# Optimization experiments

Measured on AMD Instinct MI355X. Metric: run time of the kernel, lower is better.

Reference implementation:

```python
import jax, jax.numpy as jnp
import numpy as np

B, T, D, H = 64, 1024, 1024, 1024  # batch, n_steps, n_in, n_hidden


def setup_inputs() -> dict:
    key = jax.random.key(0)
    k1, k2 = jax.random.split(key)
    x = jax.random.normal(k1, (B, T, D), dtype=jnp.float32)
    # BasicRNNCell kernel: [n_in + n_hidden, n_hidden], glorot-ish scale
    W = jax.random.normal(k2, (D + H, H), dtype=jnp.float32) * (1.0 / np.sqrt(D + H))
    b = jnp.zeros((H,), dtype=jnp.float32)
    return {"x": x, "W": W, "b": b}


def reference(x, W, b):
    """Vanilla RNN (tf BasicRNNCell): h_t = tanh([x_t, h_{t-1}] @ W + b).
    return_last=False -> outputs all hidden states, shape [B, T, H]."""
    Wx = W[: x.shape[-1]]   # [D, H]
    Wh = W[x.shape[-1]:]    # [H, H]
    # Precompute input projections for all steps in one big GEMM: [B, T, H]
    x_proj = jnp.einsum('btd,dh->bth', x, Wx) + b

    def step(h, xp_t):
        h_new = jnp.tanh(xp_t + h @ Wh)
        return h_new, h_new

    h0 = jnp.zeros((x.shape[0], Wh.shape[1]), dtype=x.dtype)
    # scan over time: [T, B, H]
    _, outs = jax.lax.scan(step, h0, jnp.swapaxes(x_proj, 0, 1))
    return jnp.swapaxes(outs, 0, 1)  # [B, T, H]
```

## Files before the change

kernel.cpp:

```cpp
#include <hip/hip_runtime.h>
#include <stdint.h>


#define T_LEN 1024
#define HID   1024

typedef float  f32x4  __attribute__((ext_vector_type(4)));
typedef __bf16 bf16x8 __attribute__((ext_vector_type(8)));
typedef unsigned long long u64;

__global__ __launch_bounds__(256) void xproj_gemm(
    const float* __restrict__ x, const float* __restrict__ W,
    const float* __restrict__ bias, float* __restrict__ out)
{
    __shared__ __align__(16) __bf16 As[128][40];
    __shared__ __align__(16) __bf16 Bs[128][40];

    const int bid = blockIdx.x;
    const int n0  = (bid & 7) << 7;
    const int64_t r0 = (int64_t)(bid >> 3) << 7;
    const int tid  = threadIdx.x;
    const int lane = tid & 63;
    const int w    = tid >> 6;
    const int hi   = lane >> 4, lo = lane & 15;
    const int wm   = (w >> 1) << 6, wn = (w & 1) << 6;

    f32x4 acc[4][4] = {};

    const int arow = tid >> 1, akh = (tid & 1) << 4;
    const int bk   = tid >> 3, bnh = (tid & 7) << 4;

    for (int k0 = 0; k0 < 1024; k0 += 32) {
        {
            const float* src = x + (r0 + arow) * 1024 + k0 + akh;
            bf16x8 t0, t1;
            #pragma unroll
            for (int i2 = 0; i2 < 8; ++i2) { t0[i2] = (__bf16)src[i2]; t1[i2] = (__bf16)src[8 + i2]; }
            *(bf16x8*)&As[arow][akh]     = t0;
            *(bf16x8*)&As[arow][akh + 8] = t1;
        }
        {
            const float* src = W + (int64_t)(k0 + bk) * 1024 + n0 + bnh;
            #pragma unroll
            for (int i2 = 0; i2 < 16; ++i2) {
                int col = bnh + i2;
                Bs[col][bk ^ (((col >> 4) & 3) << 3)] = (__bf16)src[i2];
            }
        }
        __syncthreads();

        bf16x8 af[4], bfr[4];
        #pragma unroll
        for (int f = 0; f < 4; ++f)
            af[f] = *(const bf16x8*)&As[wm + f * 16 + lo][hi << 3];
        #pragma unroll
        for (int f = 0; f < 4; ++f) {
            const int cswz = (((wn >> 4) + f) & 3) << 3;
            bfr[f] = *(const bf16x8*)&Bs[wn + f * 16 + lo][(hi << 3) ^ cswz];
        }
        #pragma unroll
        for (int fm = 0; fm < 4; ++fm)
            #pragma unroll
            for (int fn = 0; fn < 4; ++fn)
                acc[fm][fn] = __builtin_amdgcn_mfma_f32_16x16x32_bf16(af[fm], bfr[fn], acc[fm][fn], 0, 0, 0);
        __syncthreads();
    }

    #pragma unroll
    for (int fm = 0; fm < 4; ++fm) {
        const int64_t mrow = r0 + wm + fm * 16 + hi * 4;
        #pragma unroll
        for (int fn = 0; fn < 4; ++fn) {
            const int col = n0 + wn + fn * 16 + lo;
            const float bv = bias[col];
            #pragma unroll
            for (int r = 0; r < 4; ++r)
                out[(mrow + r) * 1024 + col] = acc[fm][fn][r] + bv;
        }
    }
}

__device__ __forceinline__ float tanh_fast(float x) {
    float e = __builtin_amdgcn_exp2f(x * 2.885390082f);
    return 1.0f - 2.0f * __builtin_amdgcn_rcpf(e + 1.0f);
}

__global__ __launch_bounds__(512, 2) void rnn_scan(
    const float* __restrict__ W, float* __restrict__ out,
    unsigned int* __restrict__ hx)
{
    __shared__ __align__(16) unsigned char A_lds[16 * 2048];

    const int bid = blockIdx.x;
    const int ig  = bid >> 3;
    const int jg  = bid & 7;
    const int tid = threadIdx.x;
    const int lane = tid & 63;
    const int wv  = tid >> 6;
    const int hi  = lane >> 4, lo = lane & 15;

    const int col = jg * 128 + wv * 16 + lo;
    bf16x8 breg[32];
    {
        const float* wb = W + (int64_t)1024 * 1024 + col;
        #pragma unroll
        for (int kb = 0; kb < 32; ++kb) {
            const float* src = wb + (int64_t)(kb * 32 + hi * 8) * 1024;
            bf16x8 tf;
            #pragma unroll
            for (int j = 0; j < 8; ++j) tf[j] = (__bf16)src[(int64_t)j * 1024];
            breg[kb] = tf;
        }
    }

    const int srow = tid >> 5;
    const int c32  = tid & 31;
    const int slab_u64 = (ig * 16 + srow) * 512 + c32 * 16;
    const unsigned swz_w = (unsigned)((srow & 7) << 4);
    const unsigned kbyte0 = (unsigned)(c32 * 64);

    const unsigned abase = (unsigned)(lo * 2048);
    const unsigned axor  = (unsigned)((lo & 7) << 4);

    const int64_t rstride = (int64_t)T_LEN * HID;
    float* pr0 = out + (int64_t)(ig * 16 + hi * 4) * rstride + col;
    const int wr0 = (ig * 16 + hi * 4) * 1024 + col;

    for (int t = 0; t < T_LEN; ++t) {
        float xpv0 = pr0[(int64_t)t * HID];
        float xpv1 = pr0[(int64_t)t * HID + rstride];
        float xpv2 = pr0[(int64_t)t * HID + 2 * rstride];
        float xpv3 = pr0[(int64_t)t * HID + 3 * rstride];

        f32x4 accs = {0.f, 0.f, 0.f, 0.f};
        if (t > 0) {
            const unsigned int exptag = (unsigned int)t;
            const u64* bp = (const u64*)(hx + ((t - 1) & 1) * 65536) + slab_u64;
            u64 q[16];
            #pragma unroll
            for (int j = 0; j < 16; ++j)
                q[j] = __hip_atomic_load(bp + j, __ATOMIC_RELAXED, __HIP_MEMORY_SCOPE_AGENT);
            unsigned bad = 0;
            #pragma unroll
            for (int j = 0; j < 16; ++j) {
                unsigned b = (((unsigned)(q[j] >> 16) & 0xffffu) ^ exptag)
                           | (((unsigned)(q[j] >> 48)) ^ exptag);
                bad |= (b ? 1u : 0u) << j;
            }
            while (bad) {
                __builtin_amdgcn_s_sleep(1);
                #pragma unroll
                for (int j = 0; j < 16; ++j)
                    if (bad & (1u << j)) {
                        q[j] = __hip_atomic_load(bp + j, __ATOMIC_RELAXED, __HIP_MEMORY_SCOPE_AGENT);
                        if ((((unsigned)(q[j] >> 16) & 0xffffu) == exptag) &&
                            ((unsigned)(q[j] >> 48) == exptag))
                            bad &= ~(1u << j);
                    }
            }
            unsigned dw[16];
            #pragma unroll
            for (int j = 0; j < 16; ++j)
                dw[j] = __builtin_amdgcn_perm((unsigned)(q[j] >> 32), (unsigned)q[j], 0x05040100u);
            #pragma unroll
            for (int i = 0; i < 4; ++i) {
                f32x4 v = { __builtin_bit_cast(float, dw[4 * i]),
                            __builtin_bit_cast(float, dw[4 * i + 1]),
                            __builtin_bit_cast(float, dw[4 * i + 2]),
                            __builtin_bit_cast(float, dw[4 * i + 3]) };
                *(f32x4*)(A_lds + srow * 2048 + ((kbyte0 + 16 * i) ^ swz_w)) = v;
            }
            __syncthreads();

            f32x4 acc0 = {0.f, 0.f, 0.f, 0.f}, acc1 = {0.f, 0.f, 0.f, 0.f};
            #pragma unroll
            for (int kb = 0; kb < 32; kb += 2) {
                bf16x8 a0 = *(const bf16x8*)(A_lds + abase + (((unsigned)(kb * 64) + hi * 16) ^ axor));
                bf16x8 a1 = *(const bf16x8*)(A_lds + abase + (((unsigned)((kb + 1) * 64) + hi * 16) ^ axor));
                acc0 = __builtin_amdgcn_mfma_f32_16x16x32_bf16(a0, breg[kb],     acc0, 0, 0, 0);
                acc1 = __builtin_amdgcn_mfma_f32_16x16x32_bf16(a1, breg[kb + 1], acc1, 0, 0, 0);
            }
            accs = acc0 + acc1;
        }

        float h0 = tanh_fast(xpv0 + accs[0]);
        float h1 = tanh_fast(xpv1 + accs[1]);
        float h2 = tanh_fast(xpv2 + accs[2]);
        float h3 = tanh_fast(xpv3 + accs[3]);

        unsigned int* hxs = hx + (t & 1) * 65536 + wr0;
        const unsigned int tagw = (unsigned int)(t + 1) << 16;
        __hip_atomic_store(hxs,        tagw | __builtin_bit_cast(unsigned short, (__bf16)h0),
                           __ATOMIC_RELAXED, __HIP_MEMORY_SCOPE_AGENT);
        __hip_atomic_store(hxs + 1024, tagw | __builtin_bit_cast(unsigned short, (__bf16)h1),
                           __ATOMIC_RELAXED, __HIP_MEMORY_SCOPE_AGENT);
        __hip_atomic_store(hxs + 2048, tagw | __builtin_bit_cast(unsigned short, (__bf16)h2),
                           __ATOMIC_RELAXED, __HIP_MEMORY_SCOPE_AGENT);
        __hip_atomic_store(hxs + 3072, tagw | __builtin_bit_cast(unsigned short, (__bf16)h3),
                           __ATOMIC_RELAXED, __HIP_MEMORY_SCOPE_AGENT);

        pr0[(int64_t)t * HID]               = h0;
        pr0[(int64_t)t * HID + rstride]     = h1;
        pr0[(int64_t)t * HID + 2 * rstride] = h2;
        pr0[(int64_t)t * HID + 3 * rstride] = h3;

        __syncthreads();
    }
}

extern "C" void kernel_launch(void* const* d_in, const int* in_sizes, int n_in,
                              void* d_out, int out_size, void* d_ws, size_t ws_size,
                              hipStream_t stream)
{
    const float* x    = (const float*)d_in[0];
    const float* W    = (const float*)d_in[1];
    const float* bias = (const float*)d_in[2];
    float* out = (float*)d_out;

    unsigned int* hx = (unsigned int*)d_ws;

    hipMemsetAsync(hx, 0, 524288, stream);
    xproj_gemm<<<dim3(4096), dim3(256), 0, stream>>>(x, W, bias, out);
    rnn_scan<<<dim3(32), dim3(512), 0, stream>>>(W, out, hx);
}
```

Measured before the change: 8.002 ms.

## Add per-block step flags to gate hidden-state polling and rework LDS layout

Each scan block now publishes a per-step flag after its hidden-state stores drain, and one thread spins on the 8 peer flags before the block reads the tagged hidden state. This replaces heavy per-lane polling of the data with a cheaper wait. The hidden-state LDS tile is also laid out k-major with XOR swizzling, and the MFMA reduction uses four accumulator chains. The x-projection loads move after the wait. The change adds an extra barrier and vmcnt wait per step, which lengthens the critical path of the serial recurrence.

```diff
diff --git a/kernel.cpp b/kernel.cpp
--- a/kernel.cpp
+++ b/kernel.cpp
@@ -5,8 +5,8 @@
 #define T_LEN 1024
 #define HID   1024
 
-typedef float  f32x4  __attribute__((ext_vector_type(4)));
-typedef __bf16 bf16x8 __attribute__((ext_vector_type(8)));
+typedef float    f32x4  __attribute__((ext_vector_type(4)));
+typedef __bf16   bf16x8 __attribute__((ext_vector_type(8)));
 typedef unsigned long long u64;
 
 __global__ __launch_bounds__(256) void xproj_gemm(
@@ -85,11 +85,11 @@
     return 1.0f - 2.0f * __builtin_amdgcn_rcpf(e + 1.0f);
 }
 
-__global__ __launch_bounds__(512, 2) void rnn_scan(
+__global__ __launch_bounds__(512, 1) void rnn_scan(
     const float* __restrict__ W, float* __restrict__ out,
-    unsigned int* __restrict__ hx)
+    unsigned int* hx, unsigned int* flg)
 {
-    __shared__ __align__(16) unsigned char A_lds[16 * 2048];
+    __shared__ __align__(16) unsigned char A_lds[32 * 1024];
 
     const int bid = blockIdx.x;
     const int ig  = bid >> 3;
@@ -116,71 +116,85 @@
     const int srow = tid >> 5;
     const int c32  = tid & 31;
     const int slab_u64 = (ig * 16 + srow) * 512 + c32 * 16;
-    const unsigned swz_w = (unsigned)((srow & 7) << 4);
-    const unsigned kbyte0 = (unsigned)(c32 * 64);
-
-    const unsigned abase = (unsigned)(lo * 2048);
-    const unsigned axor  = (unsigned)((lo & 7) << 4);
+    const unsigned wbase = (unsigned)(c32 * 1024);
+    const unsigned wswz  = (unsigned)(c32 & 7);
 
     const int64_t rstride = (int64_t)T_LEN * HID;
     float* pr0 = out + (int64_t)(ig * 16 + hi * 4) * rstride + col;
     const int wr0 = (ig * 16 + hi * 4) * 1024 + col;
+    const int myflag = ig * 8 + jg;
 
     for (int t = 0; t < T_LEN; ++t) {
-        float xpv0 = pr0[(int64_t)t * HID];
-        float xpv1 = pr0[(int64_t)t * HID + rstride];
-        float xpv2 = pr0[(int64_t)t * HID + 2 * rstride];
-        float xpv3 = pr0[(int64_t)t * HID + 3 * rstride];
-
         f32x4 accs = {0.f, 0.f, 0.f, 0.f};
+        float xpv0, xpv1, xpv2, xpv3;
+
         if (t > 0) {
-            const unsigned int exptag = (unsigned int)t;
+            const unsigned exptag = (unsigned)t;
+
+            if (tid == 0) {
+                const u64* fp = (const u64*)(flg + (((t - 1) & 1) * 32 + ig * 8));
+                const u64 expq = ((u64)exptag << 32) | (u64)exptag;
+                for (;;) {
+                    u64 f0 = __hip_atomic_load(fp + 0, __ATOMIC_RELAXED, __HIP_MEMORY_SCOPE_AGENT);
+                    u64 f1 = __hip_atomic_load(fp + 1, __ATOMIC_RELAXED, __HIP_MEMORY_SCOPE_AGENT);
+                    u64 f2 = __hip_atomic_load(fp + 2, __ATOMIC_RELAXED, __HIP_MEMORY_SCOPE_AGENT);
+                    u64 f3 = __hip_atomic_load(fp + 3, __ATOMIC_RELAXED, __HIP_MEMORY_SCOPE_AGENT);
+                    if (((f0 ^ expq) | (f1 ^ expq) | (f2 ^ expq) | (f3 ^ expq)) == 0) break;
+                    __builtin_amdgcn_s_sleep(1);
+                }
+            }
+            __syncthreads();
+
             const u64* bp = (const u64*)(hx + ((t - 1) & 1) * 65536) + slab_u64;
             u64 q[16];
-            #pragma unroll
-            for (int j = 0; j < 16; ++j)
-                q[j] = __hip_atomic_load(bp + j, __ATOMIC_RELAXED, __HIP_MEMORY_SCOPE_AGENT);
-            unsigned bad = 0;
-            #pragma unroll
-            for (int j = 0; j < 16; ++j) {
-                unsigned b = (((unsigned)(q[j] >> 16) & 0xffffu) ^ exptag)
-                           | (((unsigned)(q[j] >> 48)) ^ exptag);
-                bad |= (b ? 1u : 0u) << j;
-            }
-            while (bad) {
-                __builtin_amdgcn_s_sleep(1);
+            for (;;) {
                 #pragma unroll
                 for (int j = 0; j < 16; ++j)
-                    if (bad & (1u << j)) {
-                        q[j] = __hip_atomic_load(bp + j, __ATOMIC_RELAXED, __HIP_MEMORY_SCOPE_AGENT);
-                        if ((((unsigned)(q[j] >> 16) & 0xffffu) == exptag) &&
-                            ((unsigned)(q[j] >> 48) == exptag))
-                            bad &= ~(1u << j);
-                    }
-            }
-            unsigned dw[16];
+                    q[j] = __hip_atomic_load(bp + j, __ATOMIC_RELAXED, __HIP_MEMORY_SCOPE_AGENT);
+                unsigned badm = 0;
+                #pragma unroll
+                for (int j = 0; j < 16; ++j) {
+                    badm |= ((unsigned)(q[j] >> 16) & 0xffffu) ^ exptag;
+                    badm |= ((unsigned)(q[j] >> 48)) ^ exptag;
+                }
+                if (!badm) break;
+                __builtin_amdgcn_s_sleep(1);
+            }
+
+            xpv0 = pr0[(int64_t)t * HID];
+            xpv1 = pr0[(int64_t)t * HID + rstride];
+            xpv2 = pr0[(int64_t)t * HID + 2 * rstride];
+            xpv3 = pr0[(int64_t)t * HID + 3 * rstride];
+
+            unsigned dwp[16];
             #pragma unroll
             for (int j = 0; j < 16; ++j)
-                dw[j] = __builtin_amdgcn_perm((unsigned)(q[j] >> 32), (unsigned)q[j], 0x05040100u);
+                dwp[j] = __builtin_amdgcn_perm((unsigned)(q[j] >> 32), (unsigned)q[j], 0x05040100u);
             #pragma unroll
             for (int i = 0; i < 4; ++i) {
-                f32x4 v = { __builtin_bit_cast(float, dw[4 * i]),
-                            __builtin_bit_cast(float, dw[4 * i + 1]),
-                            __builtin_bit_cast(float, dw[4 * i + 2]),
-                            __builtin_bit_cast(float, dw[4 * i + 3]) };
-                *(f32x4*)(A_lds + srow * 2048 + ((kbyte0 + 16 * i) ^ swz_w)) = v;
+                f32x4 v = { __builtin_bit_cast(float, dwp[4 * i]),
+                            __builtin_bit_cast(float, dwp[4 * i + 1]),
+                            __builtin_bit_cast(float, dwp[4 * i + 2]),
+                            __builtin_bit_cast(float, dwp[4 * i + 3]) };
+                *(f32x4*)(A_lds + wbase + ((((unsigned)(i * 16 + srow)) ^ wswz) << 4)) = v;
             }
             __syncthreads();
 
-            f32x4 acc0 = {0.f, 0.f, 0.f, 0.f}, acc1 = {0.f, 0.f, 0.f, 0.f};
-            #pragma unroll
-            for (int kb = 0; kb < 32; kb += 2) {
-                bf16x8 a0 = *(const bf16x8*)(A_lds + abase + (((unsigned)(kb * 64) + hi * 16) ^ axor));
-                bf16x8 a1 = *(const bf16x8*)(A_lds + abase + (((unsigned)((kb + 1) * 64) + hi * 16) ^ axor));
-                acc0 = __builtin_amdgcn_mfma_f32_16x16x32_bf16(a0, breg[kb],     acc0, 0, 0, 0);
-                acc1 = __builtin_amdgcn_mfma_f32_16x16x32_bf16(a1, breg[kb + 1], acc1, 0, 0, 0);
-            }
-            accs = acc0 + acc1;
+            f32x4 a0 = {0.f,0.f,0.f,0.f}, a1 = a0, a2 = a0, a3 = a0;
+            #pragma unroll
+            for (int kb = 0; kb < 32; kb += 4) {
+                bf16x8 x0 = *(const bf16x8*)(A_lds + (unsigned)(kb + 0) * 1024 + ((((unsigned)lane) ^ (unsigned)((kb + 0) & 7)) << 4));
+                bf16x8 x1 = *(const bf16x8*)(A_lds + (unsigned)(kb + 1) * 1024 + ((((unsigned)lane) ^ (unsigned)((kb + 1) & 7)) << 4));
+                bf16x8 x2 = *(const bf16x8*)(A_lds + (unsigned)(kb + 2) * 1024 + ((((unsigned)lane) ^ (unsigned)((kb + 2) & 7)) << 4));
+                bf16x8 x3 = *(const bf16x8*)(A_lds + (unsigned)(kb + 3) * 1024 + ((((unsigned)lane) ^ (unsigned)((kb + 3) & 7)) << 4));
+                a0 = __builtin_amdgcn_mfma_f32_16x16x32_bf16(x0, breg[kb + 0], a0, 0, 0, 0);
+                a1 = __builtin_amdgcn_mfma_f32_16x16x32_bf16(x1, breg[kb + 1], a1, 0, 0, 0);
+                a2 = __builtin_amdgcn_mfma_f32_16x16x32_bf16(x2, breg[kb + 2], a2, 0, 0, 0);
+                a3 = __builtin_amdgcn_mfma_f32_16x16x32_bf16(x3, breg[kb + 3], a3, 0, 0, 0);
+            }
+            accs = (a0 + a1) + (a2 + a3);
+        } else {
+            xpv0 = pr0[0]; xpv1 = pr0[rstride]; xpv2 = pr0[2 * rstride]; xpv3 = pr0[3 * rstride];
         }
 
         float h0 = tanh_fast(xpv0 + accs[0]);
@@ -188,23 +202,26 @@
         float h2 = tanh_fast(xpv2 + accs[2]);
         float h3 = tanh_fast(xpv3 + accs[3]);
 
+        const unsigned tagw = (unsigned)(t + 1) << 16;
+        unsigned v0 = tagw | __builtin_bit_cast(unsigned short, (__bf16)h0);
+        unsigned v1 = tagw | __builtin_bit_cast(unsigned short, (__bf16)h1);
+        unsigned v2 = tagw | __builtin_bit_cast(unsigned short, (__bf16)h2);
+        unsigned v3 = tagw | __builtin_bit_cast(unsigned short, (__bf16)h3);
         unsigned int* hxs = hx + (t & 1) * 65536 + wr0;
-        const unsigned int tagw = (unsigned int)(t + 1) << 16;
-        __hip_atomic_store(hxs,        tagw | __builtin_bit_cast(unsigned short, (__bf16)h0),
-                           __ATOMIC_RELAXED, __HIP_MEMORY_SCOPE_AGENT);
-        __hip_atomic_store(hxs + 1024, tagw | __builtin_bit_cast(unsigned short, (__bf16)h1),
-                           __ATOMIC_RELAXED, __HIP_MEMORY_SCOPE_AGENT);
-        __hip_atomic_store(hxs + 2048, tagw | __builtin_bit_cast(unsigned short, (__bf16)h2),
-                           __ATOMIC_RELAXED, __HIP_MEMORY_SCOPE_AGENT);
-        __hip_atomic_store(hxs + 3072, tagw | __builtin_bit_cast(unsigned short, (__bf16)h3),
-                           __ATOMIC_RELAXED, __HIP_MEMORY_SCOPE_AGENT);
+        __hip_atomic_store(hxs,        v0, __ATOMIC_RELAXED, __HIP_MEMORY_SCOPE_AGENT);
+        __hip_atomic_store(hxs + 1024, v1, __ATOMIC_RELAXED, __HIP_MEMORY_SCOPE_AGENT);
+        __hip_atomic_store(hxs + 2048, v2, __ATOMIC_RELAXED, __HIP_MEMORY_SCOPE_AGENT);
+        __hip_atomic_store(hxs + 3072, v3, __ATOMIC_RELAXED, __HIP_MEMORY_SCOPE_AGENT);
+        asm volatile("s_waitcnt vmcnt(0)" ::: "memory");
+        __syncthreads();
+        if (tid == 0)
+            __hip_atomic_store(&flg[(t & 1) * 32 + myflag], (unsigned)(t + 1),
+                               __ATOMIC_RELAXED, __HIP_MEMORY_SCOPE_AGENT);
 
         pr0[(int64_t)t * HID]               = h0;
         pr0[(int64_t)t * HID + rstride]     = h1;
         pr0[(int64_t)t * HID + 2 * rstride] = h2;
         pr0[(int64_t)t * HID + 3 * rstride] = h3;
-
-        __syncthreads();
     }
 }
 
@@ -217,9 +234,10 @@
     const float* bias = (const float*)d_in[2];
     float* out = (float*)d_out;
 
-    unsigned int* hx = (unsigned int*)d_ws;
-
-    hipMemsetAsync(hx, 0, 524288, stream);
+    unsigned int* hx  = (unsigned int*)d_ws;
+    unsigned int* flg = (unsigned int*)((char*)d_ws + 524288);
+
+    (void)hipMemsetAsync(d_ws, 0, 524288 + 256, stream);
     xproj_gemm<<<dim3(4096), dim3(256), 0, stream>>>(x, W, bias, out);
-    rnn_scan<<<dim3(32), dim3(512), 0, stream>>>(W, out, hx);
-}
+    rnn_scan<<<dim3(32), dim3(512), 0, stream>>>(W, out, hx, flg);
+}
```

After: 8.490 ms. 1.06x slower.
